# Kernel tuning notes

Measured on AMD Instinct MI355X. Metric: run time of the kernel, lower is better.

Reference implementation:

```python
import jax, jax.numpy as jnp
import numpy as np

B, H, W, C = 8, 64, 64, 512
CK, CV = C // 8, C // 2  # 64, 256


def maxpool2x2(x):
    # x: [B, H, W, C] -> [B, H//2, W//2, C], 2x2 max pool, stride 2 (keras MaxPooling2D default)
    b, h, w, c = x.shape
    return x.reshape(b, h // 2, 2, w // 2, 2, c).max(axis=(2, 4))


def setup_inputs() -> dict:
    key = jax.random.key(0)
    ks = jax.random.split(key, 6)
    wscale = 0.02
    return {
        "x": jax.random.normal(ks[0], (B, H, W, C), dtype=jnp.float32),
        "w_theta": jax.random.normal(ks[1], (C, CK), dtype=jnp.float32) * wscale,
        "w_phi": jax.random.normal(ks[2], (C, CK), dtype=jnp.float32) * wscale,
        "w_g": jax.random.normal(ks[3], (C, CV), dtype=jnp.float32) * wscale,
        "w_o": jax.random.normal(ks[4], (CV, C), dtype=jnp.float32) * wscale,
        "gamma": jax.random.normal(ks[5], (1,), dtype=jnp.float32),
    }


def reference(x, w_theta, w_phi, w_g, w_o, gamma):
    b, h, w, c = x.shape
    hw = h * w
    # theta: 1x1 conv -> [B, HW, C//8]
    theta = jnp.einsum('bhwc,ck->bhwk', x, w_theta).reshape(b, hw, -1)
    # phi: 1x1 conv + 2x2 maxpool -> [B, HW//4, C//8]
    phi = maxpool2x2(jnp.einsum('bhwc,ck->bhwk', x, w_phi)).reshape(b, hw // 4, -1)
    # attention: [B, HW, HW//4], softmax over last axis
    attn = jax.nn.softmax(jnp.einsum('bqk,bpk->bqp', theta, phi), axis=-1)
    # g: 1x1 conv + 2x2 maxpool -> [B, HW//4, C//2]
    g = maxpool2x2(jnp.einsum('bhwc,cv->bhwv', x, w_g)).reshape(b, hw // 4, -1)
    # attn_g: [B, HW, C//2] -> [B, H, W, C//2] -> 1x1 conv -> [B, H, W, C]
    attn_g = jnp.einsum('bqp,bpv->bqv', attn, g).reshape(b, h, w, -1)
    attn_g = jnp.einsum('bhwv,vc->bhwc', attn_g, w_o)
    return x + gamma * attn_g
```

## Files before the change

### kernel.cpp

```cpp
#include <hip/hip_runtime.h>
#include <hip/hip_bf16.h>
#include <cstddef>
#include <cstdint>


typedef __attribute__((ext_vector_type(8))) short short8;
typedef __attribute__((ext_vector_type(4))) float float4v;

namespace {
constexpr int kB = 8, kC = 512, kCK = 64, kCV = 256, kHW = 4096, kP = 1024;
constexpr int kNP = 384;
}

__device__ __forceinline__ void gll16(const void* g, void* l) {
  __builtin_amdgcn_global_load_lds((uint32_t __attribute__((address_space(1)))*)g,
                                   (uint32_t __attribute__((address_space(3)))*)l,
                                   16, 0, 0);
}
__device__ __forceinline__ float4v mfma16(short8 a, short8 b, float4v c) {
  return __builtin_amdgcn_mfma_f32_16x16x32_bf16(a, b, c, 0, 0, 0);
}
__device__ __forceinline__ const short8* fragp(const char* tile, int row, int oct) {
  return (const short8*)(tile + row * 128 + ((oct ^ (row & 7)) * 16));
}
__device__ __forceinline__ const short8* fragp16(const char* tile, int row, int oct) {
  return (const short8*)(tile + row * 256 + ((oct ^ (row & 15)) * 16));
}

__global__ __launch_bounds__(256) void k_pack_w(
    const float* __restrict__ wt, const float* __restrict__ wphi,
    const float* __restrict__ wg, const float* __restrict__ wo,
    __hip_bfloat16* __restrict__ wAll, __hip_bfloat16* __restrict__ woT) {
  int idx = blockIdx.x * 256 + threadIdx.x;
  if (idx < 196608) {
    int n = idx >> 9, k = idx & 511;
    float v = (n < 64) ? wt[k * 64 + n]
            : (n < 128) ? wphi[k * 64 + (n - 64)]
                        : wg[k * 256 + (n - 128)];
    wAll[idx] = __float2bfloat16(v);
  } else {
    int t = idx - 196608;
    int n = t >> 8, k = t & 255;
    woT[t] = __float2bfloat16(wo[k * 512 + n]);
  }
}

__global__ __launch_bounds__(256) void k_proj(const float* __restrict__ x,
                                              const __hip_bfloat16* __restrict__ wAll,
                                              __hip_bfloat16* __restrict__ pgf) {
  __shared__ __align__(16) char smem[16384 + 49152];
  char* As = smem;
  char* Bs = smem + 16384;
  const int tid = threadIdx.x, wid = tid >> 6, lane = tid & 63;
  const int m = lane & 15, quad = lane >> 4;
  const int row0 = blockIdx.x * 64;
  const int wm = (wid >> 1) * 32, wn = (wid & 1) * 192;
  float4v acc[2][12] = {};
  for (int kc = 0; kc < 512; kc += 64) {
#pragma unroll
    for (int u = 0; u < 4; ++u) {
      const int r0 = (wid * 4 + u) * 4;
      const int row = r0 + (lane >> 4);
      const int sqg = (lane & 15) ^ (row & 15);
      gll16(x + (size_t)(row0 + row) * 512 + kc + sqg * 4, As + r0 * 256);
    }
#pragma unroll
    for (int u = 0; u < 12; ++u) {
      const int r0 = (wid * 12 + u) * 8;
      const int row = r0 + (lane >> 3);
      const int og = (lane & 7) ^ (row & 7);
      gll16(wAll + (size_t)row * 512 + kc + og * 8, Bs + r0 * 128);
    }
    __syncthreads();
#pragma unroll
    for (int kk = 0; kk < 64; kk += 32) {
      short8 af[2];
#pragma unroll
      for (int i = 0; i < 2; ++i) {
        const int row = wm + i * 16 + m;
        const int sq0 = (kk >> 2) + quad * 2;
        float4v lo = *(const float4v*)(As + row * 256 + ((sq0 ^ m) * 16));
        float4v hi = *(const float4v*)(As + row * 256 + (((sq0 + 1) ^ m) * 16));
        short8 a;
        a[0] = __builtin_bit_cast(short, __float2bfloat16(lo[0]));
        a[1] = __builtin_bit_cast(short, __float2bfloat16(lo[1]));
        a[2] = __builtin_bit_cast(short, __float2bfloat16(lo[2]));
        a[3] = __builtin_bit_cast(short, __float2bfloat16(lo[3]));
        a[4] = __builtin_bit_cast(short, __float2bfloat16(hi[0]));
        a[5] = __builtin_bit_cast(short, __float2bfloat16(hi[1]));
        a[6] = __builtin_bit_cast(short, __float2bfloat16(hi[2]));
        a[7] = __builtin_bit_cast(short, __float2bfloat16(hi[3]));
        af[i] = a;
      }
      const int oct = (kk >> 3) + quad;
#pragma unroll
      for (int j = 0; j < 12; ++j) {
        short8 bf = *fragp(Bs, wn + j * 16 + m, oct);
#pragma unroll
        for (int i = 0; i < 2; ++i) acc[i][j] = mfma16(af[i], bf, acc[i][j]);
      }
    }
    __syncthreads();
  }
#pragma unroll
  for (int i = 0; i < 2; ++i)
#pragma unroll
    for (int j = 0; j < 12; ++j)
#pragma unroll
      for (int r = 0; r < 4; ++r)
        pgf[(size_t)(row0 + wm + i * 16 + quad * 4 + r) * 384 + wn + j * 16 + m] =
            __float2bfloat16(acc[i][j][r]);
}

__global__ __launch_bounds__(256) void k_pool_phi(const __hip_bfloat16* __restrict__ pg,
                                                  __hip_bfloat16* __restrict__ phi_p) {
  int idx = blockIdx.x * 256 + threadIdx.x;
  int c = idx & 63;
  int p = (idx >> 6) & 1023;
  int b = idx >> 16;
  int ph = p >> 5, pw = p & 31;
  size_t base = ((size_t)b * 4096 + ph * 128 + pw * 2) * kNP + 64 + c;
  float v0 = __bfloat162float(pg[base]);
  float v1 = __bfloat162float(pg[base + kNP]);
  float v2 = __bfloat162float(pg[base + kNP * 64]);
  float v3 = __bfloat162float(pg[base + kNP * 64 + kNP]);
  phi_p[idx] = __float2bfloat16(fmaxf(fmaxf(v0, v1), fmaxf(v2, v3)));
}

__global__ __launch_bounds__(256) void k_pool_gT(const __hip_bfloat16* __restrict__ pg,
                                                 __hip_bfloat16* __restrict__ gT) {
  __shared__ __hip_bfloat16 t[64][65];
  const int p0 = blockIdx.x * 64, v0 = blockIdx.y * 64, b = blockIdx.z;
#pragma unroll
  for (int it = 0; it < 16; ++it) {
    int li = it * 256 + threadIdx.x;
    int pp = li >> 6, v = li & 63;
    int p = p0 + pp;
    int ph = p >> 5, pw = p & 31;
    size_t base = ((size_t)b * 4096 + ph * 128 + pw * 2) * kNP + 128 + v0 + v;
    float mv = fmaxf(
        fmaxf(__bfloat162float(pg[base]), __bfloat162float(pg[base + kNP])),
        fmaxf(__bfloat162float(pg[base + kNP * 64]), __bfloat162float(pg[base + kNP * 64 + kNP])));
    t[pp][v] = __float2bfloat16(mv);
  }
  __syncthreads();
#pragma unroll
  for (int it = 0; it < 16; ++it) {
    int li = it * 256 + threadIdx.x;
    int v = li >> 6, p = li & 63;
    gT[((size_t)b * 256 + v0 + v) * 1024 + p0 + p] = t[p][v];
  }
}

__global__ __launch_bounds__(512) void k_fattn(
    const __hip_bfloat16* __restrict__ pgf,
    const __hip_bfloat16* __restrict__ phip,
    const __hip_bfloat16* __restrict__ gT,
    __hip_bfloat16* __restrict__ O) {
  __shared__ __align__(16) char smem[65536 + 8192 + 1024 + 128];
  char* KG = smem;
  char* PQ = smem + 65536;
  float* pred = (float*)(smem + 65536 + 8192);
  float* rowstat = (float*)(smem + 65536 + 8192 + 1024);

  const int tid = threadIdx.x, wid = tid >> 6, lane = tid & 63;
  const int m = lane & 15, quad = lane >> 4;
  const int b = blockIdx.y, q0 = blockIdx.x * 32;

  if (wid < 4) {
    const int row = wid * 8 + (lane >> 3);
    const int og = (lane & 7) ^ (row & 7);
    gll16(pgf + (size_t)(b * kHW + q0 + row) * kNP + og * 8, PQ + wid * 8 * 128);
  }
  const __hip_bfloat16* phb = phip + (size_t)b * kP * 64;
  auto stageK = [&](int c, int buf) {
#pragma unroll
    for (int u = 0; u < 4; ++u) {
      const int r0 = wid * 32 + u * 8;
      const int row = r0 + (lane >> 3);
      const int og = (lane & 7) ^ (row & 7);
      gll16(phb + (size_t)(c * 256 + row) * 64 + og * 8, KG + buf * 32768 + r0 * 128);
    }
  };
  stageK(0, 0);
  __syncthreads();

  float4v sc[2][8] = {};
#pragma unroll
  for (int c = 0; c < 4; ++c) {
    if (c < 3) stageK(c + 1, (c + 1) & 1);
    const char* Kb = KG + (c & 1) * 32768;
#pragma unroll
    for (int kk = 0; kk < 64; kk += 32) {
      const int oct = (kk >> 3) + quad;
      short8 a[2], bb[2];
#pragma unroll
      for (int i = 0; i < 2; ++i) a[i] = *fragp(PQ, i * 16 + m, oct);
#pragma unroll
      for (int j = 0; j < 2; ++j) bb[j] = *fragp(Kb, wid * 32 + j * 16 + m, oct);
#pragma unroll
      for (int i = 0; i < 2; ++i)
#pragma unroll
        for (int j = 0; j < 2; ++j) sc[i][c * 2 + j] = mfma16(a[i], bb[j], sc[i][c * 2 + j]);
    }
    __syncthreads();
  }

  float mx[2][4];
#pragma unroll
  for (int i = 0; i < 2; ++i)
#pragma unroll
    for (int r = 0; r < 4; ++r) {
      float v = sc[i][0][r];
#pragma unroll
      for (int s = 1; s < 8; ++s) v = fmaxf(v, sc[i][s][r]);
#pragma unroll
      for (int d = 1; d < 16; d <<= 1) v = fmaxf(v, __shfl_xor(v, d));
      mx[i][r] = v;
    }
  if (m == 0) {
#pragma unroll
    for (int i = 0; i < 2; ++i)
#pragma unroll
      for (int r = 0; r < 4; ++r) pred[(i * 16 + quad * 4 + r) * 8 + wid] = mx[i][r];
  }
  __syncthreads();
  if (tid < 32) {
    float v = pred[tid * 8];
#pragma unroll
    for (int w = 1; w < 8; ++w) v = fmaxf(v, pred[tid * 8 + w]);
    rowstat[tid] = v;
  }
  __syncthreads();
  float sm[2][4];
#pragma unroll
  for (int i = 0; i < 2; ++i)
#pragma unroll
    for (int r = 0; r < 4; ++r) {
      const float rm = rowstat[i * 16 + quad * 4 + r];
      float s = 0.f;
#pragma unroll
      for (int ss = 0; ss < 8; ++ss) {
        float e = __expf(sc[i][ss][r] - rm);
        sc[i][ss][r] = e;
        s += e;
      }
#pragma unroll
      for (int d = 1; d < 16; d <<= 1) s += __shfl_xor(s, d);
      sm[i][r] = s;
    }
  __syncthreads();
  if (m == 0) {
#pragma unroll
    for (int i = 0; i < 2; ++i)
#pragma unroll
      for (int r = 0; r < 4; ++r) pred[(i * 16 + quad * 4 + r) * 8 + wid] = sm[i][r];
  }
  __syncthreads();
  if (tid < 32) {
    float s = 0.f;
#pragma unroll
    for (int w = 0; w < 8; ++w) s += pred[tid * 8 + w];
    rowstat[tid] = 1.f / s;
  }

  const __hip_bfloat16* gb = gT + (size_t)b * kCV * kP;
  float4v oc[2][2] = {};
  for (int cp = 0; cp < 8; ++cp) {
    __syncthreads();
#pragma unroll
    for (int u = 0; u < 8; ++u) {
      const int r0 = wid * 32 + u * 4;
      const int row = r0 + (lane >> 4);
      const int og = (lane & 15) ^ (row & 15);
      gll16(gb + (size_t)row * kP + cp * 128 + og * 8, KG + r0 * 256);
    }
    if ((wid >> 2) == (cp & 1)) {
      const int c = cp >> 1;
#pragma unroll
      for (int i = 0; i < 2; ++i)
#pragma unroll
        for (int jl = 0; jl < 2; ++jl) {
          const int pl = (wid & 3) * 32 + jl * 16 + m;
#pragma unroll
          for (int r = 0; r < 4; ++r) {
            const int row = i * 16 + quad * 4 + r;
            *(__hip_bfloat16*)(PQ + row * 256 + (((pl >> 3) ^ (row & 15)) * 16) +
                               (pl & 7) * 2) = __float2bfloat16(sc[i][c * 2 + jl][r]);
          }
        }
    }
    __syncthreads();
#pragma unroll
    for (int kk = 0; kk < 128; kk += 32) {
      const int oct = (kk >> 3) + quad;
      short8 a[2], bb[2];
#pragma unroll
      for (int i = 0; i < 2; ++i) a[i] = *fragp16(PQ, i * 16 + m, oct);
#pragma unroll
      for (int j = 0; j < 2; ++j) bb[j] = *fragp16(KG, wid * 32 + j * 16 + m, oct);
#pragma unroll
      for (int i = 0; i < 2; ++i)
#pragma unroll
        for (int j = 0; j < 2; ++j) oc[i][j] = mfma16(a[i], bb[j], oc[i][j]);
    }
  }
#pragma unroll
  for (int i = 0; i < 2; ++i)
#pragma unroll
    for (int j = 0; j < 2; ++j)
#pragma unroll
      for (int r = 0; r < 4; ++r) {
        const int row = i * 16 + quad * 4 + r;
        O[((size_t)b * kHW + q0 + row) * kCV + wid * 32 + j * 16 + m] =
            __float2bfloat16(oc[i][j][r] * rowstat[row]);
      }
}

__global__ __launch_bounds__(256) void k_out(const __hip_bfloat16* __restrict__ A,
                                             const __hip_bfloat16* __restrict__ Bw,
                                             const float* __restrict__ x,
                                             const float* __restrict__ gamma,
                                             float* __restrict__ out) {
  __shared__ __align__(16) char smem[4 * 16384];
  const int tid = threadIdx.x, wid = tid >> 6, lane = tid & 63;
  const int m = lane & 15, quad = lane >> 4;
  const int row0 = blockIdx.x * 128, col0 = blockIdx.y * 128;
  const int wm = (wid >> 1) * 64, wn = (wid & 1) * 64;
  float4v acc[4][4] = {};
  auto stage = [&](int t, int buf) {
    const int kc = t * 64;
#pragma unroll
    for (int u = 0; u < 4; ++u) {
      const int r0 = (wid * 4 + u) * 8;
      const int row = r0 + (lane >> 3);
      const int og = (lane & 7) ^ (row & 7);
      gll16(A + (size_t)(row0 + row) * 256 + kc + og * 8, smem + buf * 16384 + r0 * 128);
      gll16(Bw + (size_t)(col0 + row) * 256 + kc + og * 8,
            smem + 32768 + buf * 16384 + r0 * 128);
    }
  };
  stage(0, 0);
  __syncthreads();
#pragma unroll
  for (int t = 0; t < 4; ++t) {
    if (t < 3) stage(t + 1, (t + 1) & 1);
    const char* Ab = smem + (t & 1) * 16384;
    const char* Bb = smem + 32768 + (t & 1) * 16384;
#pragma unroll
    for (int kk = 0; kk < 64; kk += 32) {
      const int oct = (kk >> 3) + quad;
      short8 af[4], bf[4];
#pragma unroll
      for (int i = 0; i < 4; ++i) af[i] = *fragp(Ab, wm + i * 16 + m, oct);
#pragma unroll
      for (int j = 0; j < 4; ++j) bf[j] = *fragp(Bb, wn + j * 16 + m, oct);
#pragma unroll
      for (int i = 0; i < 4; ++i)
#pragma unroll
        for (int j = 0; j < 4; ++j) acc[i][j] = mfma16(af[i], bf[j], acc[i][j]);
    }
    __syncthreads();
  }
  const float g = gamma[0];
#pragma unroll
  for (int i = 0; i < 4; ++i)
#pragma unroll
    for (int j = 0; j < 4; ++j) {
      const int cc = col0 + wn + j * 16 + m;
      const int rb = row0 + wm + i * 16 + quad * 4;
#pragma unroll
      for (int r = 0; r < 4; ++r) {
        const size_t idx = (size_t)(rb + r) * 512 + cc;
        out[idx] = x[idx] + g * acc[i][j][r];
      }
    }
}

extern "C" void kernel_launch(void* const* d_in, const int* in_sizes, int n_in,
                              void* d_out, int out_size, void* d_ws, size_t ws_size,
                              hipStream_t stream) {
  (void)in_sizes; (void)n_in; (void)out_size; (void)ws_size;
  const float* x     = (const float*)d_in[0];
  const float* wt    = (const float*)d_in[1];
  const float* wphi  = (const float*)d_in[2];
  const float* wg    = (const float*)d_in[3];
  const float* wo    = (const float*)d_in[4];
  const float* gamma = (const float*)d_in[5];
  float* out = (float*)d_out;

  char* ws = (char*)d_ws;
  __hip_bfloat16* wAll = (__hip_bfloat16*)(ws);
  __hip_bfloat16* woT  = (__hip_bfloat16*)(ws + 393216);
  __hip_bfloat16* pgf  = (__hip_bfloat16*)(ws + 655360);
  __hip_bfloat16* phip = (__hip_bfloat16*)(ws + 25821184);
  __hip_bfloat16* gT   = (__hip_bfloat16*)(ws + 26869760);
  __hip_bfloat16* O    = (__hip_bfloat16*)(ws + 31064064);

  k_pack_w<<<1280, 256, 0, stream>>>(wt, wphi, wg, wo, wAll, woT);
  k_proj<<<512, 256, 0, stream>>>(x, wAll, pgf);
  k_pool_phi<<<2048, 256, 0, stream>>>(pgf, phip);
  k_pool_gT<<<dim3(16, 4, 8), 256, 0, stream>>>(pgf, gT);
  k_fattn<<<dim3(kHW / 32, kB), 512, 0, stream>>>(pgf, phip, gT, O);
  k_out<<<dim3(256, 4), 256, 0, stream>>>(O, woT, x, gamma, out);
}
```

Measured before the change: 236.7 us.

## Load attention operands straight from global into registers, store full P tile once

The fused attention kernel no longer stages Q, K and G tiles through LDS with global_load_lds and double buffering. Each wave now loads its MFMA fragments directly from global memory into registers with register double-buffering, and writes the whole 32x1024 probability tile to LDS once. That replaces the per-chunk barriers and restaging of the old loop with a single sync. The grid is flattened so consecutive blocks interleave batches, and launch bounds request higher occupancy. The output GEMM also raises wave priority around its MFMA section; the trade is uncoalesced-ish global fragment loads and more register pressure.

```diff
diff --git a/kernel.cpp b/kernel.cpp
--- a/kernel.cpp
+++ b/kernel.cpp
@@ -22,9 +22,6 @@
 }
 __device__ __forceinline__ const short8* fragp(const char* tile, int row, int oct) {
   return (const short8*)(tile + row * 128 + ((oct ^ (row & 7)) * 16));
-}
-__device__ __forceinline__ const short8* fragp16(const char* tile, int row, int oct) {
-  return (const short8*)(tile + row * 256 + ((oct ^ (row & 15)) * 16));
 }
 
 __global__ __launch_bounds__(256) void k_pack_w(
@@ -152,58 +149,48 @@
   }
 }
 
-__global__ __launch_bounds__(512) void k_fattn(
+__global__ __launch_bounds__(512, 4) void k_fattn(
     const __hip_bfloat16* __restrict__ pgf,
     const __hip_bfloat16* __restrict__ phip,
     const __hip_bfloat16* __restrict__ gT,
     __hip_bfloat16* __restrict__ O) {
-  __shared__ __align__(16) char smem[65536 + 8192 + 1024 + 128];
-  char* KG = smem;
-  char* PQ = smem + 65536;
-  float* pred = (float*)(smem + 65536 + 8192);
-  float* rowstat = (float*)(smem + 65536 + 8192 + 1024);
+  __shared__ __align__(16) char smem[65536 + 1024 + 128];
+  char* P = smem;
+  float* pred = (float*)(smem + 65536);
+  float* rowstat = (float*)(smem + 65536 + 1024);
 
   const int tid = threadIdx.x, wid = tid >> 6, lane = tid & 63;
   const int m = lane & 15, quad = lane >> 4;
-  const int b = blockIdx.y, q0 = blockIdx.x * 32;
-
-  if (wid < 4) {
-    const int row = wid * 8 + (lane >> 3);
-    const int og = (lane & 7) ^ (row & 7);
-    gll16(pgf + (size_t)(b * kHW + q0 + row) * kNP + og * 8, PQ + wid * 8 * 128);
-  }
-  const __hip_bfloat16* phb = phip + (size_t)b * kP * 64;
-  auto stageK = [&](int c, int buf) {
-#pragma unroll
-    for (int u = 0; u < 4; ++u) {
-      const int r0 = wid * 32 + u * 8;
-      const int row = r0 + (lane >> 3);
-      const int og = (lane & 7) ^ (row & 7);
-      gll16(phb + (size_t)(c * 256 + row) * 64 + og * 8, KG + buf * 32768 + r0 * 128);
-    }
-  };
-  stageK(0, 0);
-  __syncthreads();
-
+  const int bid = blockIdx.x;
+  const int b = bid & 7;
+  const int q0 = (bid >> 3) * 32;
+
+  short8 aq[2][2];
+  const __hip_bfloat16* qb = pgf + (size_t)(b * kHW + q0) * kNP;
+#pragma unroll
+  for (int i = 0; i < 2; ++i)
+#pragma unroll
+    for (int t = 0; t < 2; ++t)
+      aq[i][t] = *(const short8*)(qb + (size_t)(i * 16 + m) * kNP + t * 32 + quad * 8);
+
+  const __hip_bfloat16* kbp = phip + ((size_t)b * kP + wid * 128) * 64;
   float4v sc[2][8] = {};
-#pragma unroll
-  for (int c = 0; c < 4; ++c) {
-    if (c < 3) stageK(c + 1, (c + 1) & 1);
-    const char* Kb = KG + (c & 1) * 32768;
-#pragma unroll
-    for (int kk = 0; kk < 64; kk += 32) {
-      const int oct = (kk >> 3) + quad;
-      short8 a[2], bb[2];
-#pragma unroll
-      for (int i = 0; i < 2; ++i) a[i] = *fragp(PQ, i * 16 + m, oct);
-#pragma unroll
-      for (int j = 0; j < 2; ++j) bb[j] = *fragp(Kb, wid * 32 + j * 16 + m, oct);
-#pragma unroll
-      for (int i = 0; i < 2; ++i)
-#pragma unroll
-        for (int j = 0; j < 2; ++j) sc[i][c * 2 + j] = mfma16(a[i], bb[j], sc[i][c * 2 + j]);
-    }
-    __syncthreads();
+  short8 kf[2][2];
+#pragma unroll
+  for (int t = 0; t < 2; ++t)
+    kf[0][t] = *(const short8*)(kbp + (size_t)m * 64 + t * 32 + quad * 8);
+#pragma unroll
+  for (int c = 0; c < 8; ++c) {
+    if (c < 7) {
+#pragma unroll
+      for (int t = 0; t < 2; ++t)
+        kf[(c + 1) & 1][t] =
+            *(const short8*)(kbp + (size_t)((c + 1) * 16 + m) * 64 + t * 32 + quad * 8);
+    }
+#pragma unroll
+    for (int t = 0; t < 2; ++t)
+#pragma unroll
+      for (int i = 0; i < 2; ++i) sc[i][c] = mfma16(aq[i][t], kf[c & 1][t], sc[i][c]);
   }
 
   float mx[2][4];
@@ -264,47 +251,53 @@
     rowstat[tid] = 1.f / s;
   }
 
-  const __hip_bfloat16* gb = gT + (size_t)b * kCV * kP;
+#pragma unroll
+  for (int i = 0; i < 2; ++i)
+#pragma unroll
+    for (int c = 0; c < 8; ++c)
+#pragma unroll
+      for (int r = 0; r < 4; ++r) {
+        const int row = i * 16 + quad * 4 + r;
+        const int key = wid * 128 + c * 16 + m;
+        const int oct = (key >> 3) ^ (row & 15);
+        *(__hip_bfloat16*)(P + row * 2048 + oct * 16 + (key & 7) * 2) =
+            __float2bfloat16(sc[i][c][r]);
+      }
+  __syncthreads();
+
+  const __hip_bfloat16* gb = gT + ((size_t)b * kCV + wid * 32) * kP;
   float4v oc[2][2] = {};
-  for (int cp = 0; cp < 8; ++cp) {
-    __syncthreads();
-#pragma unroll
-    for (int u = 0; u < 8; ++u) {
-      const int r0 = wid * 32 + u * 4;
-      const int row = r0 + (lane >> 4);
-      const int og = (lane & 15) ^ (row & 15);
-      gll16(gb + (size_t)row * kP + cp * 128 + og * 8, KG + r0 * 256);
-    }
-    if ((wid >> 2) == (cp & 1)) {
-      const int c = cp >> 1;
-#pragma unroll
-      for (int i = 0; i < 2; ++i)
-#pragma unroll
-        for (int jl = 0; jl < 2; ++jl) {
-          const int pl = (wid & 3) * 32 + jl * 16 + m;
-#pragma unroll
-          for (int r = 0; r < 4; ++r) {
-            const int row = i * 16 + quad * 4 + r;
-            *(__hip_bfloat16*)(PQ + row * 256 + (((pl >> 3) ^ (row & 15)) * 16) +
-                               (pl & 7) * 2) = __float2bfloat16(sc[i][c * 2 + jl][r]);
-          }
-        }
-    }
-    __syncthreads();
-#pragma unroll
-    for (int kk = 0; kk < 128; kk += 32) {
-      const int oct = (kk >> 3) + quad;
-      short8 a[2], bb[2];
-#pragma unroll
-      for (int i = 0; i < 2; ++i) a[i] = *fragp16(PQ, i * 16 + m, oct);
-#pragma unroll
-      for (int j = 0; j < 2; ++j) bb[j] = *fragp16(KG, wid * 32 + j * 16 + m, oct);
-#pragma unroll
-      for (int i = 0; i < 2; ++i)
-#pragma unroll
-        for (int j = 0; j < 2; ++j) oc[i][j] = mfma16(a[i], bb[j], oc[i][j]);
-    }
-  }
+  short8 gf[2][2], af[2][2];
+#pragma unroll
+  for (int j = 0; j < 2; ++j)
+    gf[0][j] = *(const short8*)(gb + (size_t)(j * 16 + m) * kP + quad * 8);
+#pragma unroll
+  for (int i = 0; i < 2; ++i) {
+    const int row = i * 16 + m;
+    af[0][i] = *(const short8*)(P + row * 2048 + ((quad ^ (row & 15)) * 16));
+  }
+#pragma unroll
+  for (int cp = 0; cp < 32; ++cp) {
+    const int cur = cp & 1;
+    if (cp < 31) {
+      const int p0n = (cp + 1) * 32;
+#pragma unroll
+      for (int j = 0; j < 2; ++j)
+        gf[cur ^ 1][j] = *(const short8*)(gb + (size_t)(j * 16 + m) * kP + p0n + quad * 8);
+#pragma unroll
+      for (int i = 0; i < 2; ++i) {
+        const int row = i * 16 + m;
+        const int oct = ((cp + 1) * 4 + quad) ^ (row & 15);
+        af[cur ^ 1][i] = *(const short8*)(P + row * 2048 + oct * 16);
+      }
+    }
+#pragma unroll
+    for (int i = 0; i < 2; ++i)
+#pragma unroll
+      for (int j = 0; j < 2; ++j) oc[i][j] = mfma16(af[cur][i], gf[cur][j], oc[i][j]);
+  }
+
+  const float r0v = rowstat[quad * 4 + 0];
 #pragma unroll
   for (int i = 0; i < 2; ++i)
 #pragma unroll
@@ -315,6 +308,7 @@
         O[((size_t)b * kHW + q0 + row) * kCV + wid * 32 + j * 16 + m] =
             __float2bfloat16(oc[i][j][r] * rowstat[row]);
       }
+  (void)r0v;
 }
 
 __global__ __launch_bounds__(256) void k_out(const __hip_bfloat16* __restrict__ A,
@@ -347,6 +341,7 @@
     if (t < 3) stage(t + 1, (t + 1) & 1);
     const char* Ab = smem + (t & 1) * 16384;
     const char* Bb = smem + 32768 + (t & 1) * 16384;
+    __builtin_amdgcn_s_setprio(1);
 #pragma unroll
     for (int kk = 0; kk < 64; kk += 32) {
       const int oct = (kk >> 3) + quad;
@@ -360,6 +355,7 @@
 #pragma unroll
         for (int j = 0; j < 4; ++j) acc[i][j] = mfma16(af[i], bf[j], acc[i][j]);
     }
+    __builtin_amdgcn_s_setprio(0);
     __syncthreads();
   }
   const float g = gamma[0];
@@ -401,6 +397,6 @@
   k_proj<<<512, 256, 0, stream>>>(x, wAll, pgf);
   k_pool_phi<<<2048, 256, 0, stream>>>(pgf, phip);
   k_pool_gT<<<dim3(16, 4, 8), 256, 0, stream>>>(pgf, gT);
-  k_fattn<<<dim3(kHW / 32, kB), 512, 0, stream>>>(pgf, phip, gT, O);
+  k_fattn<<<dim3(kHW / 32 * kB), 512, 0, stream>>>(pgf, phip, gT, O);
   k_out<<<dim3(256, 4), 256, 0, stream>>>(O, woT, x, gamma, out);
 }
```

After: 256.6 us. 1.08x slower.
